# Kernel tuning notes

Measured on AMD Instinct MI355X. Metric: run time of the kernel, lower is better.

The kernel has to match this reference:

```python
import jax, jax.numpy as jnp
import numpy as np

B, T, H, W_SP, C_IN = 8, 16, 64, 64, 32
F = 64  # output_channels


def _conv(x, w):
    # x: (B,H,W,Cin), w: (kh,kw,Cin,Cout), 'same' padding, stride 1
    return jax.lax.conv_general_dilated(
        x, w, window_strides=(1, 1), padding='SAME',
        dimension_numbers=('NHWC', 'HWIO', 'NHWC'))


def setup_inputs() -> dict:
    key = jax.random.key(0)
    k1, k2, k3 = jax.random.split(key, 3)
    x = jax.random.normal(k1, (B, T, H, W_SP, C_IN), dtype=jnp.float32)
    # Keras ConvLSTM2D kernels: gates stacked [i, f, c, o] along last axis
    W = jax.random.normal(k2, (3, 3, C_IN, 4 * F), dtype=jnp.float32) * 0.05
    U = jax.random.normal(k3, (3, 3, F, 4 * F), dtype=jnp.float32) * 0.05
    b = jnp.zeros((4 * F,), dtype=jnp.float32)
    return {"x": x, "W": W, "U": U, "b": b}


def reference(x, W, U, b):
    # ConvLSTM2D: activation='relu', recurrent_activation='hard_sigmoid',
    # return_sequences=False -> final hidden state (B,H,W,F)
    rec_act = jax.nn.hard_sigmoid  # relu6(x+3)/6
    act = jax.nn.relu

    h0 = jnp.zeros((x.shape[0], x.shape[2], x.shape[3], F), dtype=x.dtype)
    c0 = jnp.zeros_like(h0)

    def step(carry, x_t):
        h, c = carry
        z = _conv(x_t, W) + _conv(h, U) + b  # (B,H,W,4F)
        zi, zf, zc, zo = jnp.split(z, 4, axis=-1)
        i = rec_act(zi)
        f = rec_act(zf)
        o = rec_act(zo)
        c_new = f * c + i * act(zc)
        h_new = o * act(c_new)
        return (h_new, c_new), None

    xs = jnp.transpose(x, (1, 0, 2, 3, 4))  # (T,B,H,W,Cin)
    (h_final, _), _ = jax.lax.scan(step, (h0, c0), xs)
    return h_final
```

## Files before the change

### kernel.cpp

```cpp
#include <hip/hip_runtime.h>


#define TSTEPS 16

typedef short bf16x8 __attribute__((ext_vector_type(8)));
typedef float f32x4 __attribute__((ext_vector_type(4)));
typedef unsigned int __attribute__((address_space(1))) gu32;
typedef unsigned int __attribute__((address_space(3))) lu32;

__device__ __forceinline__ float hsig(float x) {
    return fminf(fmaxf((x + 3.0f) * (1.0f / 6.0f), 0.0f), 1.0f);
}

__device__ __forceinline__ unsigned short f2bf(float f) {
    union { float f; unsigned int u; } v; v.f = f;
    unsigned int r = v.u + 0x7fffu + ((v.u >> 16) & 1u);
    return (unsigned short)(r >> 16);
}

__global__ __launch_bounds__(256)
void prepack_w(const float* __restrict__ Wg, const float* __restrict__ Ug,
               unsigned short* __restrict__ out)
{
    int idx = blockIdx.x * 256 + threadIdx.x;
    if (idx >= 27648) return;
    int lane = idx & 63;
    int nt   = (idx >> 6) & 15;
    int s    = idx >> 10;
    int col = lane & 15, quad = lane >> 4;
    int n = nt * 16 + col;
    int k0 = quad * 8;
    const float* src;
    if (s < 9) {
        src = Wg + ((size_t)s * 32 + k0) * 256 + n;
    } else {
        int ss = s - 9; int tap = ss >> 1; int half = ss & 1;
        src = Ug + ((size_t)tap * 64 + half * 32 + k0) * 256 + n;
    }
    unsigned short tmp[8];
    #pragma unroll
    for (int j = 0; j < 8; ++j) tmp[j] = f2bf(src[(size_t)j * 256]);
    *(uint4*)(out + (size_t)idx * 8) = *(uint4*)tmp;
}

template<int NS>
__global__ __launch_bounds__(512)
__attribute__((amdgpu_waves_per_eu(2, 2)))
void convlstm_step(const float* __restrict__ x,
                   const unsigned short* __restrict__ wpk,
                   const float* __restrict__ bias,
                   const unsigned short* __restrict__ h_in,
                   float* __restrict__ c_st,
                   unsigned short* __restrict__ h_out,
                   int t, int is_last)
{
    constexpr bool HP = (NS == 27);
    constexpr int  P  = 6;

    __shared__ __align__(16) unsigned short xs_s[180 * 40];
    __shared__ __align__(16) unsigned short hs_s[HP ? 180 * 72 : 8];
    __shared__ __align__(16) unsigned short bring[P * 16 * 512];

    const int tid = threadIdx.x;
    const int bid  = blockIdx.x;
    const int b    = bid & 7;
    const int tile = bid >> 3;
    const int gx0  = (tile & 7) * 8;
    const int gy0  = (tile >> 3) * 16;

    const int lane  = tid & 63;
    const int w     = tid >> 6;
    const int pxgrp = w >> 2;
    const int ngrp  = w & 3;
    const int quad  = lane >> 4;
    const int m     = lane & 15;
    const int ch    = ngrp * 16 + m;

    auto issueDMA = [&](int s) {
        int slot = s % P;
        #pragma unroll
        for (int g = 0; g < 2; ++g) {
            int nt = w + 8 * g;
            const unsigned short* gp = wpk + ((size_t)(s * 16 + nt) * 64 + lane) * 8;
            unsigned short* lp = bring + ((size_t)slot * 16 + nt) * 512;
            __builtin_amdgcn_global_load_lds((const gu32*)gp, (lu32*)lp, 16, 0, 0);
        }
    };

    issueDMA(0);
    issueDMA(1);
    issueDMA(2);

    uint4 hv0 = make_uint4(0u,0u,0u,0u), hv1 = make_uint4(0u,0u,0u,0u),
          hv2 = make_uint4(0u,0u,0u,0u);
    int ho0 = 0, ho1 = 0, ho2 = -1;
    if constexpr (HP) {
        const unsigned short* hb = h_in + ((size_t)b * (64 * 64 * 64));
        auto issueH = [&](int idx, uint4& v, int& off) {
            int pix = idx >> 3, q = idx & 7;
            int iy = pix / 10, ix = pix - iy * 10;
            int gy = gy0 + iy - 1, gx = gx0 + ix - 1;
            if ((unsigned)gy < 64u && (unsigned)gx < 64u)
                v = *(const uint4*)(hb + ((size_t)(gy * 64 + gx) * 64) + q * 8);
            off = pix * 72 + q * 8;
        };
        issueH(tid,        hv0, ho0);
        issueH(tid + 512,  hv1, ho1);
        if (tid < 416) issueH(tid + 1024, hv2, ho2);
    }

    {
        const float* xt = x + (((size_t)b * TSTEPS + t) * (size_t)(64 * 64 * 32));
        #pragma unroll 3
        for (int idx = tid; idx < 180 * 8; idx += 512) {
            int pix = idx >> 3, q = idx & 7;
            int iy = pix / 10, ix = pix - iy * 10;
            int gy = gy0 + iy - 1, gx = gx0 + ix - 1;
            unsigned short o[4] = {0, 0, 0, 0};
            if ((unsigned)gy < 64u && (unsigned)gx < 64u) {
                float4 v = *(const float4*)(xt + ((size_t)(gy * 64 + gx) * 32) + q * 4);
                o[0] = f2bf(v.x); o[1] = f2bf(v.y); o[2] = f2bf(v.z); o[3] = f2bf(v.w);
            }
            *(ushort4*)(xs_s + pix * 40 + q * 4) = *(ushort4*)o;
        }
    }
    __syncthreads();

    int xb[4], hb_[4];
    #pragma unroll
    for (int mt = 0; mt < 4; ++mt) {
        int p = mt * 16 + m;
        int row = pxgrp * 8 + (p >> 3);
        int cc  = p & 7;
        xb[mt]  = (row * 10 + cc) * 40 + quad * 8;
        hb_[mt] = (row * 10 + cc) * 72 + quad * 8;
    }

    f32x4 acc[4][4];
    #pragma unroll
    for (int g = 0; g < 4; ++g) {
        float bv = bias[g * 64 + ch];
        f32x4 bi = (f32x4){bv, bv, bv, bv};
        #pragma unroll
        for (int mt = 0; mt < 4; ++mt) acc[mt][g] = bi;
    }

    float cpre[4][4];
    if constexpr (!HP) {
        #pragma unroll
        for (int mt = 0; mt < 4; ++mt)
            #pragma unroll
            for (int r = 0; r < 4; ++r) cpre[mt][r] = 0.0f;
    }

    #pragma unroll
    for (int g0 = 0; g0 < NS; g0 += 3) {
        if (g0 + 3 < NS) { issueDMA(g0 + 3); issueDMA(g0 + 4); issueDMA(g0 + 5); }

        if constexpr (HP) {
            if (g0 == 18) {
                #pragma unroll
                for (int mt = 0; mt < 4; ++mt)
                    #pragma unroll
                    for (int r = 0; r < 4; ++r) {
                        int p = mt * 16 + quad * 4 + r;
                        int py = pxgrp * 8 + (p >> 3), px = p & 7;
                        size_t gidx = (((size_t)b * 64 + (gy0 + py)) * 64 + (gx0 + px)) * 64 + ch;
                        cpre[mt][r] = c_st[gidx];
                    }
            }
        }

        #pragma unroll
        for (int j = 0; j < 3; ++j) {
            const int s = g0 + j;
            const int slot = s % P;

            bf16x8 bfr[4];
            #pragma unroll
            for (int g = 0; g < 4; ++g)
                bfr[g] = *(const bf16x8*)(bring + ((size_t)slot * 16 + (ngrp + 4 * g)) * 512 + lane * 8);

            bf16x8 a[4];
            if (s < 9) {
                int taplin = (s / 3) * 10 + (s % 3);
                #pragma unroll
                for (int mt = 0; mt < 4; ++mt)
                    a[mt] = *(const bf16x8*)(xs_s + xb[mt] + taplin * 40);
            } else {
                int ss = s - 9, tap = ss >> 1, half = ss & 1;
                int taplin = (tap / 3) * 10 + (tap % 3);
                #pragma unroll
                for (int mt = 0; mt < 4; ++mt)
                    a[mt] = *(const bf16x8*)(hs_s + hb_[mt] + taplin * 72 + half * 32);
            }

            #pragma unroll
            for (int g = 0; g < 4; ++g)
                #pragma unroll
                for (int mt = 0; mt < 4; ++mt)
                    acc[mt][g] = __builtin_amdgcn_mfma_f32_16x16x32_bf16(a[mt], bfr[g], acc[mt][g], 0, 0, 0);
        }

        if constexpr (HP) {
            if (g0 == 6) {
                *(uint4*)(hs_s + ho0) = hv0;
                *(uint4*)(hs_s + ho1) = hv1;
                if (ho2 >= 0) *(uint4*)(hs_s + ho2) = hv2;
            }
        }

        __syncthreads();
    }

    #pragma unroll
    for (int mt = 0; mt < 4; ++mt) {
        #pragma unroll
        for (int r = 0; r < 4; ++r) {
            int p = mt * 16 + quad * 4 + r;
            int py = pxgrp * 8 + (p >> 3), px = p & 7;
            size_t gidx = (((size_t)b * 64 + (gy0 + py)) * 64 + (gx0 + px)) * 64 + ch;
            float zi = acc[mt][0][r];
            float zf = acc[mt][1][r];
            float zc = acc[mt][2][r];
            float zo = acc[mt][3][r];
            float cn = hsig(zf) * cpre[mt][r] + hsig(zi) * fmaxf(zc, 0.0f);
            float hn = hsig(zo) * fmaxf(cn, 0.0f);
            if (is_last) {
                c_st[gidx] = hn;
            } else {
                c_st[gidx] = cn;
                h_out[gidx] = f2bf(hn);
            }
        }
    }
}

extern "C" void kernel_launch(void* const* d_in, const int* in_sizes, int n_in,
                              void* d_out, int out_size, void* d_ws, size_t ws_size,
                              hipStream_t stream) {
    const float* x  = (const float*)d_in[0];
    const float* Wg = (const float*)d_in[1];
    const float* Ug = (const float*)d_in[2];
    const float* bs = (const float*)d_in[3];

    unsigned short* wpk = (unsigned short*)d_ws;
    unsigned short* h0  = (unsigned short*)((char*)d_ws + 27 * 16 * 64 * 8 * 2);
    unsigned short* h1  = h0 + (size_t)8 * 64 * 64 * 64;
    float* cS = (float*)d_out;

    prepack_w<<<108, 256, 0, stream>>>(Wg, Ug, wpk);

    dim3 grid(256);
    dim3 block(512);
    for (int t = 0; t < TSTEPS; ++t) {
        const unsigned short* hin = (t == 0) ? h0 : ((t & 1) ? h0 : h1);
        unsigned short* hout = (t & 1) ? h1 : h0;
        if (t == 0) {
            convlstm_step<9><<<grid, block, 0, stream>>>(x, wpk, bs, hin, cS, hout, t, 0);
        } else {
            convlstm_step<27><<<grid, block, 0, stream>>>(x, wpk, bs, hin, cS, hout,
                                                          t, (t == TSTEPS - 1) ? 1 : 0);
        }
    }
}
```

Measured before the change: 365.0 us.

## Double block to 1024 threads, load weights directly to registers, stage gates via LDS

Doubles the threads per block so each wave computes two gate column tiles instead of four. The LDS weight ring and its async global-to-LDS DMA go away; weights are prefetched into registers one tap ahead, straight from global/L2. The gate combine now goes through a shared-memory z buffer that reuses the input staging area, so each thread processes whole cells with all four gates. The aim is more waves per CU for latency hiding and lower LDS use, at the cost of extra barriers and repeated global weight reads.

```diff
diff --git a/kernel.cpp b/kernel.cpp
--- a/kernel.cpp
+++ b/kernel.cpp
@@ -5,8 +5,6 @@
 
 typedef short bf16x8 __attribute__((ext_vector_type(8)));
 typedef float f32x4 __attribute__((ext_vector_type(4)));
-typedef unsigned int __attribute__((address_space(1))) gu32;
-typedef unsigned int __attribute__((address_space(3))) lu32;
 
 __device__ __forceinline__ float hsig(float x) {
     return fminf(fmaxf((x + 3.0f) * (1.0f / 6.0f), 0.0f), 1.0f);
@@ -44,8 +42,8 @@
 }
 
 template<int NS>
-__global__ __launch_bounds__(512)
-__attribute__((amdgpu_waves_per_eu(2, 2)))
+__global__ __launch_bounds__(1024)
+__attribute__((amdgpu_waves_per_eu(4, 4)))
 void convlstm_step(const float* __restrict__ x,
                    const unsigned short* __restrict__ wpk,
                    const float* __restrict__ bias,
@@ -55,13 +53,13 @@
                    int t, int is_last)
 {
     constexpr bool HP = (NS == 27);
-    constexpr int  P  = 6;
-
-    __shared__ __align__(16) unsigned short xs_s[180 * 40];
-    __shared__ __align__(16) unsigned short hs_s[HP ? 180 * 72 : 8];
-    __shared__ __align__(16) unsigned short bring[P * 16 * 512];
-
-    const int tid = threadIdx.x;
+
+    __shared__ __align__(16) unsigned char smem[40320];
+    unsigned short* xs_s = (unsigned short*)smem;
+    unsigned short* hs_s = (unsigned short*)(smem + 14400);
+    float*          zbuf = (float*)smem;
+
+    const int tid  = threadIdx.x;
     const int bid  = blockIdx.x;
     const int b    = bid & 7;
     const int tile = bid >> 3;
@@ -70,30 +68,13 @@
 
     const int lane  = tid & 63;
     const int w     = tid >> 6;
-    const int pxgrp = w >> 2;
-    const int ngrp  = w & 3;
+    const int pxgrp = w >> 3;
+    const int ngrp  = w & 7;
     const int quad  = lane >> 4;
     const int m     = lane & 15;
-    const int ch    = ngrp * 16 + m;
-
-    auto issueDMA = [&](int s) {
-        int slot = s % P;
-        #pragma unroll
-        for (int g = 0; g < 2; ++g) {
-            int nt = w + 8 * g;
-            const unsigned short* gp = wpk + ((size_t)(s * 16 + nt) * 64 + lane) * 8;
-            unsigned short* lp = bring + ((size_t)slot * 16 + nt) * 512;
-            __builtin_amdgcn_global_load_lds((const gu32*)gp, (lu32*)lp, 16, 0, 0);
-        }
-    };
-
-    issueDMA(0);
-    issueDMA(1);
-    issueDMA(2);
-
-    uint4 hv0 = make_uint4(0u,0u,0u,0u), hv1 = make_uint4(0u,0u,0u,0u),
-          hv2 = make_uint4(0u,0u,0u,0u);
-    int ho0 = 0, ho1 = 0, ho2 = -1;
+
+    uint4 hv0 = make_uint4(0u,0u,0u,0u), hv1 = make_uint4(0u,0u,0u,0u);
+    int ho0 = 0, ho1 = -1;
     if constexpr (HP) {
         const unsigned short* hb = h_in + ((size_t)b * (64 * 64 * 64));
         auto issueH = [&](int idx, uint4& v, int& off) {
@@ -104,15 +85,14 @@
                 v = *(const uint4*)(hb + ((size_t)(gy * 64 + gx) * 64) + q * 8);
             off = pix * 72 + q * 8;
         };
-        issueH(tid,        hv0, ho0);
-        issueH(tid + 512,  hv1, ho1);
-        if (tid < 416) issueH(tid + 1024, hv2, ho2);
+        issueH(tid, hv0, ho0);
+        if (tid < 416) issueH(tid + 1024, hv1, ho1);
     }
 
     {
         const float* xt = x + (((size_t)b * TSTEPS + t) * (size_t)(64 * 64 * 32));
-        #pragma unroll 3
-        for (int idx = tid; idx < 180 * 8; idx += 512) {
+        #pragma unroll 2
+        for (int idx = tid; idx < 180 * 8; idx += 1024) {
             int pix = idx >> 3, q = idx & 7;
             int iy = pix / 10, ix = pix - iy * 10;
             int gy = gy0 + iy - 1, gx = gx0 + ix - 1;
@@ -136,96 +116,108 @@
         hb_[mt] = (row * 10 + cc) * 72 + quad * 8;
     }
 
-    f32x4 acc[4][4];
-    #pragma unroll
-    for (int g = 0; g < 4; ++g) {
-        float bv = bias[g * 64 + ch];
+    f32x4 acc[4][2];
+    #pragma unroll
+    for (int g = 0; g < 2; ++g) {
+        float bv = bias[(2 * ngrp + g) * 16 + m];
         f32x4 bi = (f32x4){bv, bv, bv, bv};
         #pragma unroll
         for (int mt = 0; mt < 4; ++mt) acc[mt][g] = bi;
     }
 
-    float cpre[4][4];
+    float cpre[4][2];
     if constexpr (!HP) {
         #pragma unroll
-        for (int mt = 0; mt < 4; ++mt)
-            #pragma unroll
-            for (int r = 0; r < 4; ++r) cpre[mt][r] = 0.0f;
-    }
-
-    #pragma unroll
-    for (int g0 = 0; g0 < NS; g0 += 3) {
-        if (g0 + 3 < NS) { issueDMA(g0 + 3); issueDMA(g0 + 4); issueDMA(g0 + 5); }
+        for (int q = 0; q < 4; ++q) { cpre[q][0] = 0.0f; cpre[q][1] = 0.0f; }
+    }
+
+    auto loadB = [&](int s, bf16x8* dst) {
+        #pragma unroll
+        for (int g = 0; g < 2; ++g)
+            dst[g] = *(const bf16x8*)(wpk + ((size_t)(s * 16 + 2 * ngrp + g) * 64 + lane) * 8);
+    };
+
+    bf16x8 bC[2], bN[2];
+    loadB(0, bC);
+
+    #pragma unroll
+    for (int s = 0; s < NS; ++s) {
+        if (s + 1 < NS) loadB(s + 1, bN);
+
+        bf16x8 a[4];
+        if (s < 9) {
+            int taplin = (s / 3) * 10 + (s % 3);
+            #pragma unroll
+            for (int mt = 0; mt < 4; ++mt)
+                a[mt] = *(const bf16x8*)(xs_s + xb[mt] + taplin * 40);
+        } else {
+            int ss = s - 9, tap = ss >> 1, half = ss & 1;
+            int taplin = (tap / 3) * 10 + (tap % 3);
+            #pragma unroll
+            for (int mt = 0; mt < 4; ++mt)
+                a[mt] = *(const bf16x8*)(hs_s + hb_[mt] + taplin * 72 + half * 32);
+        }
+
+        #pragma unroll
+        for (int g = 0; g < 2; ++g)
+            #pragma unroll
+            for (int mt = 0; mt < 4; ++mt)
+                acc[mt][g] = __builtin_amdgcn_mfma_f32_16x16x32_bf16(a[mt], bC[g], acc[mt][g], 0, 0, 0);
+
+        #pragma unroll
+        for (int i = 0; i < 2; ++i) bC[i] = bN[i];
 
         if constexpr (HP) {
-            if (g0 == 18) {
+            if (s == 8) {
+                *(uint4*)(hs_s + ho0) = hv0;
+                if (ho1 >= 0) *(uint4*)(hs_s + ho1) = hv1;
+                __syncthreads();
+            }
+            if (s == 17) {
                 #pragma unroll
-                for (int mt = 0; mt < 4; ++mt)
+                for (int q = 0; q < 4; ++q)
+                    #pragma unroll
+                    for (int j = 0; j < 2; ++j) {
+                        int cell = tid + j * 1024;
+                        int pl = cell >> 6, fch = cell & 63;
+                        int row = q * 4 + (pl >> 3), col = pl & 7;
+                        size_t gidx = (((size_t)b * 64 + (gy0 + row)) * 64 + (gx0 + col)) * 64 + fch;
+                        cpre[q][j] = c_st[gidx];
+                    }
+            }
+        }
+    }
+
+    __syncthreads();
+    #pragma unroll
+    for (int q = 0; q < 4; ++q) {
+        if (q) __syncthreads();
+        if (pxgrp == (q >> 1)) {
+            #pragma unroll
+            for (int mtl = 0; mtl < 2; ++mtl) {
+                int mt = 2 * (q & 1) + mtl;
+                #pragma unroll
+                for (int g = 0; g < 2; ++g)
                     #pragma unroll
                     for (int r = 0; r < 4; ++r) {
                         int p = mt * 16 + quad * 4 + r;
-                        int py = pxgrp * 8 + (p >> 3), px = p & 7;
-                        size_t gidx = (((size_t)b * 64 + (gy0 + py)) * 64 + (gx0 + px)) * 64 + ch;
-                        cpre[mt][r] = c_st[gidx];
+                        int rowl = (p >> 3) - (q & 1) * 4;
+                        int pl = rowl * 8 + (p & 7);
+                        int n = (2 * ngrp + g) * 16 + m;
+                        zbuf[((pl * 64) + (n & 63)) * 4 + (n >> 6)] = acc[mt][g][r];
                     }
             }
         }
-
-        #pragma unroll
-        for (int j = 0; j < 3; ++j) {
-            const int s = g0 + j;
-            const int slot = s % P;
-
-            bf16x8 bfr[4];
-            #pragma unroll
-            for (int g = 0; g < 4; ++g)
-                bfr[g] = *(const bf16x8*)(bring + ((size_t)slot * 16 + (ngrp + 4 * g)) * 512 + lane * 8);
-
-            bf16x8 a[4];
-            if (s < 9) {
-                int taplin = (s / 3) * 10 + (s % 3);
-                #pragma unroll
-                for (int mt = 0; mt < 4; ++mt)
-                    a[mt] = *(const bf16x8*)(xs_s + xb[mt] + taplin * 40);
-            } else {
-                int ss = s - 9, tap = ss >> 1, half = ss & 1;
-                int taplin = (tap / 3) * 10 + (tap % 3);
-                #pragma unroll
-                for (int mt = 0; mt < 4; ++mt)
-                    a[mt] = *(const bf16x8*)(hs_s + hb_[mt] + taplin * 72 + half * 32);
-            }
-
-            #pragma unroll
-            for (int g = 0; g < 4; ++g)
-                #pragma unroll
-                for (int mt = 0; mt < 4; ++mt)
-                    acc[mt][g] = __builtin_amdgcn_mfma_f32_16x16x32_bf16(a[mt], bfr[g], acc[mt][g], 0, 0, 0);
-        }
-
-        if constexpr (HP) {
-            if (g0 == 6) {
-                *(uint4*)(hs_s + ho0) = hv0;
-                *(uint4*)(hs_s + ho1) = hv1;
-                if (ho2 >= 0) *(uint4*)(hs_s + ho2) = hv2;
-            }
-        }
-
         __syncthreads();
-    }
-
-    #pragma unroll
-    for (int mt = 0; mt < 4; ++mt) {
-        #pragma unroll
-        for (int r = 0; r < 4; ++r) {
-            int p = mt * 16 + quad * 4 + r;
-            int py = pxgrp * 8 + (p >> 3), px = p & 7;
-            size_t gidx = (((size_t)b * 64 + (gy0 + py)) * 64 + (gx0 + px)) * 64 + ch;
-            float zi = acc[mt][0][r];
-            float zf = acc[mt][1][r];
-            float zc = acc[mt][2][r];
-            float zo = acc[mt][3][r];
-            float cn = hsig(zf) * cpre[mt][r] + hsig(zi) * fmaxf(zc, 0.0f);
-            float hn = hsig(zo) * fmaxf(cn, 0.0f);
+        #pragma unroll
+        for (int j = 0; j < 2; ++j) {
+            int cell = tid + j * 1024;
+            int pl = cell >> 6, fch = cell & 63;
+            int row = q * 4 + (pl >> 3), col = pl & 7;
+            float4 z = *(const float4*)(zbuf + (size_t)cell * 4);
+            size_t gidx = (((size_t)b * 64 + (gy0 + row)) * 64 + (gx0 + col)) * 64 + fch;
+            float cn = hsig(z.y) * cpre[q][j] + hsig(z.x) * fmaxf(z.z, 0.0f);
+            float hn = hsig(z.w) * fmaxf(cn, 0.0f);
             if (is_last) {
                 c_st[gidx] = hn;
             } else {
@@ -252,7 +244,7 @@
     prepack_w<<<108, 256, 0, stream>>>(Wg, Ug, wpk);
 
     dim3 grid(256);
-    dim3 block(512);
+    dim3 block(1024);
     for (int t = 0; t < TSTEPS; ++t) {
         const unsigned short* hin = (t == 0) ? h0 : ((t & 1) ? h0 : h1);
         unsigned short* hout = (t & 1) ? h1 : h0;
```

Result: slower. 383.3 us (+5.0%).
